# Kernel tuning notes

Measured on AMD Instinct MI355X. Metric: run time of the kernel, lower is better.

## Reference

```python
import jax, jax.numpy as jnp
import numpy as np

VOXEL_SIZE = 0.1
EPS = 1e-5  # torch BatchNorm1d default eps
P1, P2, P3 = 73856093, 19349663, 83492791  # spatial hash primes


def _bn_gelu(x, g, b):
    # BatchNorm1d in training mode (batch stats, biased variance) + exact GELU
    m = x.mean(0)
    v = ((x - m) ** 2).mean(0)
    return jax.nn.gelu(g * (x - m) * jax.lax.rsqrt(v + EPS) + b, approximate=False)


def setup_inputs() -> dict:
    key = jax.random.key(0)
    ks = jax.random.split(key, 6)
    B, N, D = 4, 65536, 128
    return {
        "points": jax.random.normal(ks[0], (B, N, 3), jnp.float32) * 4.0,
        "w1": jax.random.normal(ks[1], (3, D), jnp.float32) * (3 ** -0.5),
        "g1": jnp.ones((D,), jnp.float32), "b1": jnp.zeros((D,), jnp.float32),
        "w2": jax.random.normal(ks[2], (D, D), jnp.float32) * (D ** -0.5),
        "g2": jnp.ones((D,), jnp.float32), "b2": jnp.zeros((D,), jnp.float32),
        "w3": jax.random.normal(ks[3], (D + 6, D), jnp.float32) * ((D + 6) ** -0.5),
        "g3": jnp.ones((D,), jnp.float32), "b3": jnp.zeros((D,), jnp.float32),
        "w4": jax.random.normal(ks[4], (D, D), jnp.float32) * (D ** -0.5),
        "g4": jnp.ones((D,), jnp.float32), "b4": jnp.zeros((D,), jnp.float32),
    }


def reference(points, w1, g1, b1, w2, g2, b2, w3, g3, b3, w4, g4, b4):
    B, N, _ = points.shape
    P = B * N  # target_size in the torch module
    pts = points.reshape(P, 3)

    # --- hash-based voxel grouping (voxel_pooling_torch) ---
    vidx = jnp.floor(pts / VOXEL_SIZE).astype(jnp.int32)           # (P,3)
    vhash = vidx[:, 0] * P1 + vidx[:, 1] * P2 + vidx[:, 2] * P3    # (P,)
    _, inv = jnp.unique(vhash, return_inverse=True, size=P,
                        fill_value=jnp.iinfo(jnp.int32).min)       # inv: (P,)

    counts = jax.ops.segment_sum(jnp.ones((P,), pts.dtype), inv, num_segments=P)
    denom = jnp.maximum(counts, 1.0)[:, None]
    # scatter_reduce 'mean' over points; empty (padded) voxel slots stay 0,
    # matching pad_tensor(fill_value=0)
    voxel_centroids = jax.ops.segment_sum(pts, inv, num_segments=P) / denom  # (P,3)
    pooled_features = voxel_centroids  # features == flat_points, mean pooling

    # unique voxel coords with batch index, padded with -1 (pad_tensor fill=-1)
    batch_idx = jnp.repeat(jnp.arange(B, dtype=jnp.int32), N)
    uvox = jnp.full((P, 4), -1, jnp.int32).at[inv].set(
        jnp.concatenate([batch_idx[:, None], vidx], axis=1))
    uvox = jnp.where(counts[:, None] > 0, uvox, -1)

    # --- centroid normalization + MLPs ---
    norm_points = pts - voxel_centroids[inv]                        # (P,3)
    pe = _bn_gelu(norm_points @ w1, g1, b1)
    pos_embs = _bn_gelu(pe @ w2, g2, b2)                            # (P,D)

    concat = jnp.concatenate([pts, pos_embs, pooled_features], axis=1)  # (P,D+6)
    af = _bn_gelu(concat @ w3, g3, b3)
    aggregated = _bn_gelu(af @ w4, g4, b4)                          # (P,D)

    # sparse COO tensor represented as (indices, values)
    return aggregated, uvox.T, norm_points
```

## Files before the change

### kernel.cpp

```cpp
#include <hip/hip_runtime.h>
#include <cstddef>

#define EPSBN 1e-5f

typedef __attribute__((ext_vector_type(8))) short bf16x8;
typedef __attribute__((ext_vector_type(4))) float f32x4;

__device__ __forceinline__ float gelu_f(float x) {
    return 0.5f * x * (1.0f + erff(x * 0.70710678118654752440f));
}

__device__ __forceinline__ float bfu2f(unsigned short u) {
    unsigned v = ((unsigned)u) << 16;
    return __uint_as_float(v);
}

__device__ __forceinline__ unsigned short f2bfu(float f) {
    unsigned u = __float_as_uint(f);
    unsigned r = (u + 0x7fffu + ((u >> 16) & 1u)) >> 16;
    return (unsigned short)r;
}

__device__ __forceinline__ int swz_byte(int byte, int r) {
    return (byte < 256) ? (byte ^ ((r & 7) << 4)) : byte;
}

__device__ __forceinline__ void voxel_idx(const float* __restrict__ pts, int i,
                                          int& vx, int& vy, int& vz) {
    float x = pts[i * 3 + 0], y = pts[i * 3 + 1], z = pts[i * 3 + 2];
    vx = (int)floorf(x / 0.1f);
    vy = (int)floorf(y / 0.1f);
    vz = (int)floorf(z / 0.1f);
}

__device__ __forceinline__ unsigned flip_hash(const float* __restrict__ pts, int i) {
    int vx, vy, vz;
    voxel_idx(pts, i, vx, vy, vz);
    unsigned h = (unsigned)vx * 73856093u + (unsigned)vy * 19349663u + (unsigned)vz * 83492791u;
    return h ^ 0x80000000u;
}

__global__ void fill_f32(float* p, float v, int n) {
    int i = blockIdx.x * blockDim.x + threadIdx.x;
    if (i < n) p[i] = v;
}

__global__ void key_kernel(const float* __restrict__ pts, int* __restrict__ key,
                           int* __restrict__ cnt, int P) {
    int i = blockIdx.x * blockDim.x + threadIdx.x;
    if (i >= P) return;
    unsigned fk = flip_hash(pts, i);
    key[i] = (int)fk;
    atomicAdd(&cnt[fk >> 16], 1);
}

__global__ void scanA(const int* __restrict__ in, int* __restrict__ out, int* __restrict__ bsum) {
    __shared__ int s[256];
    int tid = threadIdx.x;
    int i = blockIdx.x * 256 + tid;
    int v = in[i];
    s[tid] = v;
    __syncthreads();
    for (int off = 1; off < 256; off <<= 1) {
        int t = (tid >= off) ? s[tid - off] : 0;
        __syncthreads();
        s[tid] += t;
        __syncthreads();
    }
    out[i] = s[tid] - v;
    if (tid == 255) bsum[blockIdx.x] = s[255];
}

__global__ void scanB(int* bsum) {
    __shared__ int s[256];
    int tid = threadIdx.x;
    int v = bsum[tid];
    s[tid] = v;
    __syncthreads();
    for (int off = 1; off < 256; off <<= 1) {
        int t = (tid >= off) ? s[tid - off] : 0;
        __syncthreads();
        s[tid] += t;
        __syncthreads();
    }
    bsum[tid] = s[tid] - v;
}

__global__ void scanC(int* __restrict__ out, const int* __restrict__ bsum) {
    out[blockIdx.x * 256 + threadIdx.x] += bsum[blockIdx.x];
}

__global__ void scatter_kernel(const int* __restrict__ key, const int* __restrict__ off,
                               int* __restrict__ fill, int* __restrict__ lo, int P) {
    int i = blockIdx.x * blockDim.x + threadIdx.x;
    if (i >= P) return;
    unsigned fk = (unsigned)key[i];
    int hi = fk >> 16;
    int pos = off[hi] + atomicAdd(&fill[hi], 1);
    lo[pos] = (int)(fk & 0xFFFFu);
}

__global__ void bucket_unique(const int* __restrict__ off, const int* __restrict__ cnt,
                              int* __restrict__ lo, int* __restrict__ dcnt, int NB) {
    int b = blockIdx.x * blockDim.x + threadIdx.x;
    if (b >= NB) return;
    int n = cnt[b];
    int base = off[b];
    if (n == 0) { dcnt[b] = 0; return; }
    for (int j = 0; j < n - 1; ++j) {
        int mi = j, mv = lo[base + j];
        for (int k = j + 1; k < n; ++k) {
            int v = lo[base + k];
            if (v < mv) { mv = v; mi = k; }
        }
        if (mi != j) { lo[base + mi] = lo[base + j]; lo[base + j] = mv; }
    }
    int d = 0, prev = -1;
    for (int j = 0; j < n; ++j) {
        int v = lo[base + j];
        if (j == 0 || v != prev) lo[base + d++] = v;
        prev = v;
    }
    dcnt[b] = d;
}

__global__ void rank_kernel(const int* __restrict__ key, const int* __restrict__ off,
                            const int* __restrict__ dcnt, const int* __restrict__ lo,
                            const int* __restrict__ dpre, int* __restrict__ inv, int P) {
    int i = blockIdx.x * blockDim.x + threadIdx.x;
    if (i >= P) return;
    unsigned fk = (unsigned)key[i];
    int hi = fk >> 16;
    int l = (int)(fk & 0xFFFFu);
    int base = off[hi];
    int d = dcnt[hi];
    int r = 0;
    for (int j = 0; j < d; ++j) {
        if (lo[base + j] == l) { r = j; break; }
    }
    inv[i] = dpre[hi] + r;
}

__global__ void accum_kernel(const float* __restrict__ pts, const int* __restrict__ inv,
                             float* __restrict__ counts, float* __restrict__ csum,
                             int* __restrict__ winner, int P) {
    int i = blockIdx.x * blockDim.x + threadIdx.x;
    if (i >= P) return;
    int s = inv[i];
    atomicAdd(&counts[s], 1.0f);
    atomicAdd(&csum[s * 3 + 0], pts[i * 3 + 0]);
    atomicAdd(&csum[s * 3 + 1], pts[i * 3 + 1]);
    atomicAdd(&csum[s * 3 + 2], pts[i * 3 + 2]);
    atomicMax(&winner[s], i);
}

__global__ void centroid_kernel(float* __restrict__ csum, const float* __restrict__ counts, int P) {
    int s = blockIdx.x * blockDim.x + threadIdx.x;
    if (s >= P) return;
    float d = fmaxf(counts[s], 1.0f);
    csum[s * 3 + 0] /= d;
    csum[s * 3 + 1] /= d;
    csum[s * 3 + 2] /= d;
}

__global__ void uvox_norm_kernel(const float* __restrict__ pts, const int* __restrict__ inv,
                                 const int* __restrict__ winner, const float* __restrict__ cent,
                                 float* __restrict__ out2, float* __restrict__ out3,
                                 int P, int N) {
    int i = blockIdx.x * blockDim.x + threadIdx.x;
    if (i >= P) return;
    int s = inv[i];
    float px = pts[i * 3 + 0], py = pts[i * 3 + 1], pz = pts[i * 3 + 2];
    out3[i * 3 + 0] = px - cent[s * 3 + 0];
    out3[i * 3 + 1] = py - cent[s * 3 + 1];
    out3[i * 3 + 2] = pz - cent[s * 3 + 2];
    if (winner[s] == i) {
        out2[0 * (size_t)P + s] = (float)(i / N);
        out2[1 * (size_t)P + s] = (float)(int)floorf(px / 0.1f);
        out2[2 * (size_t)P + s] = (float)(int)floorf(py / 0.1f);
        out2[3 * (size_t)P + s] = (float)(int)floorf(pz / 0.1f);
    }
}

__global__ void l1stats(const float* __restrict__ norm, const float* __restrict__ w1g,
                        float* __restrict__ spart, int P) {
    int c = threadIdx.x;
    int row0 = blockIdx.x * 64;
    float w0 = w1g[c], wa = w1g[128 + c], wb = w1g[256 + c];
    float s = 0.f, q = 0.f;
    for (int r = 0; r < 64; ++r) {
        const float* nr = norm + (size_t)(row0 + r) * 3;
        float v = nr[0] * w0 + nr[1] * wa + nr[2] * wb;
        s += v;
        q += v * v;
    }
    int b = blockIdx.x & 63;
    atomicAdd(&spart[b * 256 + c], s);
    atomicAdd(&spart[b * 256 + 128 + c], q);
}

__global__ void finalize_bn(const float* __restrict__ spart, const float* __restrict__ g,
                            const float* __restrict__ b, float* __restrict__ prm, int P) {
    int c = threadIdx.x;
    float s = 0.f, q = 0.f;
    for (int t = 0; t < 64; ++t) {
        s += spart[t * 256 + c];
        q += spart[t * 256 + 128 + c];
    }
    float m = s / (float)P;
    float var = fmaxf(q / (float)P - m * m, 0.f);
    float A = g[c] * rsqrtf(var + EPSBN);
    prm[c] = A;
    prm[128 + c] = b[c] - A * m;
}

__global__ void prep_wt(const float* __restrict__ w2, const float* __restrict__ w3,
                        const float* __restrict__ w4, unsigned short* __restrict__ wt2,
                        unsigned short* __restrict__ wt3, unsigned short* __restrict__ wt4) {
    int t = blockIdx.x * 256 + threadIdx.x;
    if (t < 16384) {
        int n = t >> 7, k = t & 127;
        wt2[n * 128 + k] = f2bfu(w2[k * 128 + n]);
    } else if (t < 16384 + 20480) {
        int u = t - 16384;
        int n = u / 160, k = u - n * 160;
        float v = 0.f;
        if (k < 134) {
            int r = (k < 128) ? (k + 3) : ((k < 131) ? (k - 128) : k);
            v = w3[r * 128 + n];
        }
        wt3[n * 160 + k] = f2bfu(v);
    } else if (t < 53248) {
        int u = t - 36864;
        int n = u >> 7, k = u & 127;
        wt4[n * 128 + k] = f2bfu(w4[k * 128 + n]);
    }
}

template <int KPAD, int MODE>
__launch_bounds__(256, 2)
__global__ void gemm_layer(const unsigned short* __restrict__ act_raw,
                           const float* __restrict__ norm,
                           const float* __restrict__ w1g,
                           const float* __restrict__ prm,
                           const float* __restrict__ pts,
                           const float* __restrict__ cent,
                           const unsigned short* __restrict__ wt,
                           unsigned short* __restrict__ out_raw,
                           float* __restrict__ spart, int P) {
    __shared__ __align__(16) unsigned short sA[64 * KPAD];
    const int tid = threadIdx.x;
    const int row0 = blockIdx.x * 64;

    for (int e = tid * 4; e < 64 * 128; e += 1024) {
        int r = e >> 7, k = e & 127;
        float v0, v1, v2, v3;
        if constexpr (MODE == 1) {
            const float* nr = norm + (size_t)(row0 + r) * 3;
            float n0 = nr[0], n1 = nr[1], n2 = nr[2];
            float r0 = n0 * w1g[k + 0] + n1 * w1g[128 + k + 0] + n2 * w1g[256 + k + 0];
            float r1 = n0 * w1g[k + 1] + n1 * w1g[128 + k + 1] + n2 * w1g[256 + k + 1];
            float r2 = n0 * w1g[k + 2] + n1 * w1g[128 + k + 2] + n2 * w1g[256 + k + 2];
            float r3 = n0 * w1g[k + 3] + n1 * w1g[128 + k + 3] + n2 * w1g[256 + k + 3];
            float4 pA = *(const float4*)&prm[k];
            float4 pB = *(const float4*)&prm[128 + k];
            v0 = gelu_f(pA.x * r0 + pB.x);
            v1 = gelu_f(pA.y * r1 + pB.y);
            v2 = gelu_f(pA.z * r2 + pB.z);
            v3 = gelu_f(pA.w * r3 + pB.w);
        } else {
            ushort4 rv = *(const ushort4*)&act_raw[(size_t)(row0 + r) * 128 + k];
            float4 pA = *(const float4*)&prm[k];
            float4 pB = *(const float4*)&prm[128 + k];
            v0 = gelu_f(pA.x * bfu2f(rv.x) + pB.x);
            v1 = gelu_f(pA.y * bfu2f(rv.y) + pB.y);
            v2 = gelu_f(pA.z * bfu2f(rv.z) + pB.z);
            v3 = gelu_f(pA.w * bfu2f(rv.w) + pB.w);
        }
        unsigned lo = (unsigned)f2bfu(v0) | ((unsigned)f2bfu(v1) << 16);
        unsigned hi = (unsigned)f2bfu(v2) | ((unsigned)f2bfu(v3) << 16);
        *(uint2*)((char*)sA + r * (KPAD * 2) + swz_byte(k * 2, r)) = make_uint2(lo, hi);
    }
    if constexpr (MODE == 2) {
        for (int t = tid; t < 64 * 8; t += 256) {
            int r = t >> 3, ch = t & 7;
            float a = 0.f, b = 0.f, c = 0.f, d = 0.f;
            if (ch == 0) {
                a = pts[(size_t)(row0 + r) * 3 + 0];
                b = pts[(size_t)(row0 + r) * 3 + 1];
                c = pts[(size_t)(row0 + r) * 3 + 2];
                d = cent[(size_t)(row0 + r) * 3 + 0];
            } else if (ch == 1) {
                a = cent[(size_t)(row0 + r) * 3 + 1];
                b = cent[(size_t)(row0 + r) * 3 + 2];
            }
            unsigned lo = (unsigned)f2bfu(a) | ((unsigned)f2bfu(b) << 16);
            unsigned hi = (unsigned)f2bfu(c) | ((unsigned)f2bfu(d) << 16);
            int byte = swz_byte((128 + ch * 4) * 2, r);
            *(uint2*)((char*)sA + r * (KPAD * 2) + byte) = make_uint2(lo, hi);
        }
    }
    __syncthreads();

    const int lane = tid & 63;
    const int wid = tid >> 6;
    const int lrow = lane & 15;
    const int kg = lane >> 4;

    const unsigned short* wbase = wt + (size_t)(wid * 32 + lrow) * KPAD + kg * 8;

    f32x4 acc[4][2] = {};
#pragma unroll
    for (int ks = 0; ks < KPAD / 32; ++ks) {
        bf16x8 a[4], b[2];
        int kbyte = ks * 64 + kg * 16;
#pragma unroll
        for (int j = 0; j < 2; ++j)
            b[j] = *(const bf16x8*)(wbase + (size_t)j * 16 * KPAD + ks * 32);
#pragma unroll
        for (int i = 0; i < 4; ++i) {
            int r = i * 16 + lrow;
            a[i] = *(const bf16x8*)((const char*)sA + r * (KPAD * 2) + swz_byte(kbyte, r));
        }
#pragma unroll
        for (int i = 0; i < 4; ++i)
#pragma unroll
            for (int j = 0; j < 2; ++j)
                acc[i][j] = __builtin_amdgcn_mfma_f32_16x16x32_bf16(a[i], b[j], acc[i][j], 0, 0, 0);
    }

    float s[2] = {0.f, 0.f}, q[2] = {0.f, 0.f};
#pragma unroll
    for (int i = 0; i < 4; ++i) {
        int rbase = row0 + i * 16 + kg * 4;
#pragma unroll
        for (int j = 0; j < 2; ++j) {
            int col = wid * 32 + j * 16 + lrow;
#pragma unroll
            for (int reg = 0; reg < 4; ++reg) {
                float v = acc[i][j][reg];
                out_raw[(size_t)(rbase + reg) * 128 + col] = f2bfu(v);
                s[j] += v;
                q[j] += v * v;
            }
        }
    }

    __syncthreads();
    float* red = (float*)sA;
    red[tid] = 0.f;
    __syncthreads();
#pragma unroll
    for (int j = 0; j < 2; ++j) {
        int col = wid * 32 + j * 16 + lrow;
        atomicAdd(&red[col], s[j]);
        atomicAdd(&red[128 + col], q[j]);
    }
    __syncthreads();
    atomicAdd(&spart[(blockIdx.x & 63) * 256 + tid], red[tid]);
}

__global__ void bn_gelu_out(const unsigned short* __restrict__ raw, const float* __restrict__ prm,
                            float* __restrict__ out, int n) {
    int i = blockIdx.x * blockDim.x + threadIdx.x;
    int idx4 = i * 4;
    if (idx4 >= n) return;
    ushort4 v = *(const ushort4*)&raw[idx4];
    int c = idx4 & 127;
    float4 o;
    o.x = gelu_f(prm[c + 0] * bfu2f(v.x) + prm[128 + c + 0]);
    o.y = gelu_f(prm[c + 1] * bfu2f(v.y) + prm[128 + c + 1]);
    o.z = gelu_f(prm[c + 2] * bfu2f(v.z) + prm[128 + c + 2]);
    o.w = gelu_f(prm[c + 3] * bfu2f(v.w) + prm[128 + c + 3]);
    *(float4*)&out[idx4] = o;
}

extern "C" void kernel_launch(void* const* d_in, const int* in_sizes, int n_in,
                              void* d_out, int out_size, void* d_ws, size_t ws_size,
                              hipStream_t stream) {
    const float* pts = (const float*)d_in[0];
    const float* w1 = (const float*)d_in[1];
    const float* g1 = (const float*)d_in[2];
    const float* b1 = (const float*)d_in[3];
    const float* w2 = (const float*)d_in[4];
    const float* g2 = (const float*)d_in[5];
    const float* b2 = (const float*)d_in[6];
    const float* w3 = (const float*)d_in[7];
    const float* g3 = (const float*)d_in[8];
    const float* b3 = (const float*)d_in[9];
    const float* w4 = (const float*)d_in[10];
    const float* g4 = (const float*)d_in[11];
    const float* b4 = (const float*)d_in[12];

    const int P = in_sizes[0] / 3;
    const int N = P / 4;
    const int NB = 65536;

    float* out0 = (float*)d_out;
    float* out2 = out0 + (size_t)P * 128;
    float* out3 = out2 + (size_t)P * 4;

    char* ws = (char*)d_ws;
    size_t P4 = (size_t)P * 4;
    int* d_key = (int*)(ws + 0 * P4);
    int* d_lo = (int*)(ws + 1 * P4);
    int* d_inv = (int*)(ws + 2 * P4);
    float* d_counts = (float*)(ws + 3 * P4);
    float* d_csum = (float*)(ws + 4 * P4);
    int* d_winner = (int*)(ws + 7 * P4);
    char* base8 = ws + 8 * P4;
    int* d_cnt = (int*)(base8);
    int* d_off = (int*)(base8 + 1 * 262144);
    int* d_fill = (int*)(base8 + 2 * 262144);
    int* d_dcnt = (int*)(base8 + 3 * 262144);
    int* d_dpre = (int*)(base8 + 4 * 262144);
    float* d_stats = (float*)(base8 + 5 * 262144);
    float* d_params = (float*)(base8 + 6 * 262144);
    int* d_bsum = (int*)(base8 + 6 * 262144 + 16384);
    unsigned short* d_wt2 = (unsigned short*)(base8 + 6 * 262144 + 65536);
    unsigned short* d_wt3 = d_wt2 + 128 * 128;
    unsigned short* d_wt4 = d_wt3 + 128 * 160;
    char* bufbase = base8 + 6 * 262144 + 65536 + 262144;
    unsigned short* d_bufA = (unsigned short*)bufbase;
    unsigned short* d_bufB = (unsigned short*)(bufbase + (size_t)P * 128 * 2);

    const int nb = (P + 255) / 256;

    (void)hipMemsetAsync(d_cnt, 0, 262144, stream);
    (void)hipMemsetAsync(d_fill, 0, 262144, stream);
    (void)hipMemsetAsync(d_counts, 0, P4, stream);
    (void)hipMemsetAsync(d_csum, 0, 3 * P4, stream);
    (void)hipMemsetAsync(d_winner, 0xFF, P4, stream);
    (void)hipMemsetAsync(d_stats, 0, 262144, stream);
    fill_f32<<<(4 * P + 255) / 256, 256, 0, stream>>>(out2, -1.0f, 4 * P);

    key_kernel<<<nb, 256, 0, stream>>>(pts, d_key, d_cnt, P);
    scanA<<<256, 256, 0, stream>>>(d_cnt, d_off, d_bsum);
    scanB<<<1, 256, 0, stream>>>(d_bsum);
    scanC<<<256, 256, 0, stream>>>(d_off, d_bsum);
    scatter_kernel<<<nb, 256, 0, stream>>>(d_key, d_off, d_fill, d_lo, P);
    bucket_unique<<<NB / 256, 256, 0, stream>>>(d_off, d_cnt, d_lo, d_dcnt, NB);
    scanA<<<256, 256, 0, stream>>>(d_dcnt, d_dpre, d_bsum);
    scanB<<<1, 256, 0, stream>>>(d_bsum);
    scanC<<<256, 256, 0, stream>>>(d_dpre, d_bsum);
    rank_kernel<<<nb, 256, 0, stream>>>(d_key, d_off, d_dcnt, d_lo, d_dpre, d_inv, P);

    accum_kernel<<<nb, 256, 0, stream>>>(pts, d_inv, d_counts, d_csum, d_winner, P);
    centroid_kernel<<<nb, 256, 0, stream>>>(d_csum, d_counts, P);
    uvox_norm_kernel<<<nb, 256, 0, stream>>>(pts, d_inv, d_winner, d_csum, out2, out3, P, N);

    prep_wt<<<208, 256, 0, stream>>>(w2, w3, w4, d_wt2, d_wt3, d_wt4);

    l1stats<<<P / 64, 128, 0, stream>>>(out3, w1, d_stats, P);
    finalize_bn<<<1, 128, 0, stream>>>(d_stats, g1, b1, d_params, P);

    gemm_layer<128, 1><<<P / 64, 256, 0, stream>>>(
        nullptr, out3, w1, d_params, nullptr, nullptr, d_wt2, d_bufA, d_stats + 1 * 64 * 256, P);
    finalize_bn<<<1, 128, 0, stream>>>(d_stats + 1 * 64 * 256, g2, b2, d_params + 256, P);

    gemm_layer<160, 2><<<P / 64, 256, 0, stream>>>(
        d_bufA, nullptr, nullptr, d_params + 256, pts, d_csum, d_wt3, d_bufB, d_stats + 2 * 64 * 256, P);
    finalize_bn<<<1, 128, 0, stream>>>(d_stats + 2 * 64 * 256, g3, b3, d_params + 512, P);

    gemm_layer<128, 0><<<P / 64, 256, 0, stream>>>(
        d_bufB, nullptr, nullptr, d_params + 512, nullptr, nullptr, d_wt4, d_bufA, d_stats + 3 * 64 * 256, P);
    finalize_bn<<<1, 128, 0, stream>>>(d_stats + 3 * 64 * 256, g4, b4, d_params + 768, P);

    bn_gelu_out<<<(P * 128 / 4 + 255) / 256, 256, 0, stream>>>(
        d_bufA, d_params + 768, out0, P * 128);
}
```

Baseline: 581.8 us.

## Fuse voxel preprocessing kernels and replace three-pass scans with single-block scan

Folds the -1 fill of the voxel-coordinate output into the hashing kernel, merges rank lookup with the centroid atomics, and merges centroid normalization with the layer-1 BN statistics using shared memory. The three-kernel hierarchical scans become a single 1024-thread block scan, and the separate memsets are coalesced into fewer calls. This cuts launch count and extra global round trips over the point arrays. In exchange, the single-block scan serializes 64 elements per thread, and the fused stats kernel assumes P is a multiple of 256.

```diff
diff --git a/kernel.cpp b/kernel.cpp
--- a/kernel.cpp
+++ b/kernel.cpp
@@ -25,69 +25,47 @@
     return (byte < 256) ? (byte ^ ((r & 7) << 4)) : byte;
 }
 
-__device__ __forceinline__ void voxel_idx(const float* __restrict__ pts, int i,
-                                          int& vx, int& vy, int& vz) {
-    float x = pts[i * 3 + 0], y = pts[i * 3 + 1], z = pts[i * 3 + 2];
-    vx = (int)floorf(x / 0.1f);
-    vy = (int)floorf(y / 0.1f);
-    vz = (int)floorf(z / 0.1f);
-}
-
-__device__ __forceinline__ unsigned flip_hash(const float* __restrict__ pts, int i) {
-    int vx, vy, vz;
-    voxel_idx(pts, i, vx, vy, vz);
+__device__ __forceinline__ unsigned flip_hash3(float x, float y, float z) {
+    int vx = (int)floorf(x / 0.1f);
+    int vy = (int)floorf(y / 0.1f);
+    int vz = (int)floorf(z / 0.1f);
     unsigned h = (unsigned)vx * 73856093u + (unsigned)vy * 19349663u + (unsigned)vz * 83492791u;
     return h ^ 0x80000000u;
 }
 
-__global__ void fill_f32(float* p, float v, int n) {
-    int i = blockIdx.x * blockDim.x + threadIdx.x;
-    if (i < n) p[i] = v;
-}
-
-__global__ void key_kernel(const float* __restrict__ pts, int* __restrict__ key,
-                           int* __restrict__ cnt, int P) {
+__global__ void key_fill_kernel(const float* __restrict__ pts, int* __restrict__ key,
+                                int* __restrict__ cnt, float* __restrict__ out2, int P) {
     int i = blockIdx.x * blockDim.x + threadIdx.x;
     if (i >= P) return;
-    unsigned fk = flip_hash(pts, i);
+    unsigned fk = flip_hash3(pts[i * 3 + 0], pts[i * 3 + 1], pts[i * 3 + 2]);
     key[i] = (int)fk;
     atomicAdd(&cnt[fk >> 16], 1);
-}
-
-__global__ void scanA(const int* __restrict__ in, int* __restrict__ out, int* __restrict__ bsum) {
-    __shared__ int s[256];
+    out2[0 * (size_t)P + i] = -1.0f;
+    out2[1 * (size_t)P + i] = -1.0f;
+    out2[2 * (size_t)P + i] = -1.0f;
+    out2[3 * (size_t)P + i] = -1.0f;
+}
+
+__global__ void scan_ex(const int* __restrict__ in, int* __restrict__ out, int n) {
+    __shared__ int s[1024];
     int tid = threadIdx.x;
-    int i = blockIdx.x * 256 + tid;
-    int v = in[i];
-    s[tid] = v;
-    __syncthreads();
-    for (int off = 1; off < 256; off <<= 1) {
+    int beg = tid * 64;
+    int sum = 0;
+    for (int i = 0; i < 64; ++i) sum += in[beg + i];
+    s[tid] = sum;
+    __syncthreads();
+    for (int off = 1; off < 1024; off <<= 1) {
         int t = (tid >= off) ? s[tid - off] : 0;
         __syncthreads();
         s[tid] += t;
         __syncthreads();
     }
-    out[i] = s[tid] - v;
-    if (tid == 255) bsum[blockIdx.x] = s[255];
-}
-
-__global__ void scanB(int* bsum) {
-    __shared__ int s[256];
-    int tid = threadIdx.x;
-    int v = bsum[tid];
-    s[tid] = v;
-    __syncthreads();
-    for (int off = 1; off < 256; off <<= 1) {
-        int t = (tid >= off) ? s[tid - off] : 0;
-        __syncthreads();
-        s[tid] += t;
-        __syncthreads();
-    }
-    bsum[tid] = s[tid] - v;
-}
-
-__global__ void scanC(int* __restrict__ out, const int* __restrict__ bsum) {
-    out[blockIdx.x * 256 + threadIdx.x] += bsum[blockIdx.x];
+    int base = s[tid] - sum;
+    for (int i = 0; i < 64; ++i) {
+        int v = in[beg + i];
+        out[beg + i] = base;
+        base += v;
+    }
 }
 
 __global__ void scatter_kernel(const int* __restrict__ key, const int* __restrict__ off,
@@ -124,9 +102,11 @@
     dcnt[b] = d;
 }
 
-__global__ void rank_kernel(const int* __restrict__ key, const int* __restrict__ off,
-                            const int* __restrict__ dcnt, const int* __restrict__ lo,
-                            const int* __restrict__ dpre, int* __restrict__ inv, int P) {
+__global__ void rank_accum_kernel(const int* __restrict__ key, const int* __restrict__ off,
+                                  const int* __restrict__ dcnt, const int* __restrict__ lo,
+                                  const int* __restrict__ dpre, const float* __restrict__ pts,
+                                  int* __restrict__ inv, float* __restrict__ counts,
+                                  float* __restrict__ csum, int* __restrict__ winner, int P) {
     int i = blockIdx.x * blockDim.x + threadIdx.x;
     if (i >= P) return;
     unsigned fk = (unsigned)key[i];
@@ -138,15 +118,8 @@
     for (int j = 0; j < d; ++j) {
         if (lo[base + j] == l) { r = j; break; }
     }
-    inv[i] = dpre[hi] + r;
-}
-
-__global__ void accum_kernel(const float* __restrict__ pts, const int* __restrict__ inv,
-                             float* __restrict__ counts, float* __restrict__ csum,
-                             int* __restrict__ winner, int P) {
-    int i = blockIdx.x * blockDim.x + threadIdx.x;
-    if (i >= P) return;
-    int s = inv[i];
+    int s = dpre[hi] + r;
+    inv[i] = s;
     atomicAdd(&counts[s], 1.0f);
     atomicAdd(&csum[s * 3 + 0], pts[i * 3 + 0]);
     atomicAdd(&csum[s * 3 + 1], pts[i * 3 + 1]);
@@ -163,40 +136,46 @@
     csum[s * 3 + 2] /= d;
 }
 
-__global__ void uvox_norm_kernel(const float* __restrict__ pts, const int* __restrict__ inv,
-                                 const int* __restrict__ winner, const float* __restrict__ cent,
-                                 float* __restrict__ out2, float* __restrict__ out3,
-                                 int P, int N) {
-    int i = blockIdx.x * blockDim.x + threadIdx.x;
-    if (i >= P) return;
+__global__ void uvox_norm_l1_kernel(const float* __restrict__ pts, const int* __restrict__ inv,
+                                    const int* __restrict__ winner, const float* __restrict__ cent,
+                                    const float* __restrict__ w1g, float* __restrict__ out2,
+                                    float* __restrict__ out3, float* __restrict__ spart,
+                                    int P, int N) {
+    __shared__ float sn[256 * 3];
+    int tid = threadIdx.x;
+    int i = blockIdx.x * 256 + tid;
     int s = inv[i];
     float px = pts[i * 3 + 0], py = pts[i * 3 + 1], pz = pts[i * 3 + 2];
-    out3[i * 3 + 0] = px - cent[s * 3 + 0];
-    out3[i * 3 + 1] = py - cent[s * 3 + 1];
-    out3[i * 3 + 2] = pz - cent[s * 3 + 2];
+    float n0 = px - cent[s * 3 + 0];
+    float n1 = py - cent[s * 3 + 1];
+    float n2 = pz - cent[s * 3 + 2];
+    out3[i * 3 + 0] = n0;
+    out3[i * 3 + 1] = n1;
+    out3[i * 3 + 2] = n2;
     if (winner[s] == i) {
         out2[0 * (size_t)P + s] = (float)(i / N);
         out2[1 * (size_t)P + s] = (float)(int)floorf(px / 0.1f);
         out2[2 * (size_t)P + s] = (float)(int)floorf(py / 0.1f);
         out2[3 * (size_t)P + s] = (float)(int)floorf(pz / 0.1f);
     }
-}
-
-__global__ void l1stats(const float* __restrict__ norm, const float* __restrict__ w1g,
-                        float* __restrict__ spart, int P) {
-    int c = threadIdx.x;
-    int row0 = blockIdx.x * 64;
+    sn[tid * 3 + 0] = n0;
+    sn[tid * 3 + 1] = n1;
+    sn[tid * 3 + 2] = n2;
+    __syncthreads();
+    int c = tid & 127;
+    int h = tid >> 7;
     float w0 = w1g[c], wa = w1g[128 + c], wb = w1g[256 + c];
-    float s = 0.f, q = 0.f;
-    for (int r = 0; r < 64; ++r) {
-        const float* nr = norm + (size_t)(row0 + r) * 3;
-        float v = nr[0] * w0 + nr[1] * wa + nr[2] * wb;
-        s += v;
-        q += v * v;
+    float ssum = 0.f, qsum = 0.f;
+    int r0 = h * 128;
+    for (int r = 0; r < 128; ++r) {
+        int row = r0 + r;
+        float v = sn[row * 3 + 0] * w0 + sn[row * 3 + 1] * wa + sn[row * 3 + 2] * wb;
+        ssum += v;
+        qsum += v * v;
     }
     int b = blockIdx.x & 63;
-    atomicAdd(&spart[b * 256 + c], s);
-    atomicAdd(&spart[b * 256 + 128 + c], q);
+    atomicAdd(&spart[b * 256 + c], ssum);
+    atomicAdd(&spart[b * 256 + 128 + c], qsum);
 }
 
 __global__ void finalize_bn(const float* __restrict__ spart, const float* __restrict__ g,
@@ -410,13 +389,12 @@
     int* d_winner = (int*)(ws + 7 * P4);
     char* base8 = ws + 8 * P4;
     int* d_cnt = (int*)(base8);
-    int* d_off = (int*)(base8 + 1 * 262144);
-    int* d_fill = (int*)(base8 + 2 * 262144);
+    int* d_fill = (int*)(base8 + 1 * 262144);
+    int* d_off = (int*)(base8 + 2 * 262144);
     int* d_dcnt = (int*)(base8 + 3 * 262144);
     int* d_dpre = (int*)(base8 + 4 * 262144);
     float* d_stats = (float*)(base8 + 5 * 262144);
     float* d_params = (float*)(base8 + 6 * 262144);
-    int* d_bsum = (int*)(base8 + 6 * 262144 + 16384);
     unsigned short* d_wt2 = (unsigned short*)(base8 + 6 * 262144 + 65536);
     unsigned short* d_wt3 = d_wt2 + 128 * 128;
     unsigned short* d_wt4 = d_wt3 + 128 * 160;
@@ -426,32 +404,24 @@
 
     const int nb = (P + 255) / 256;
 
-    (void)hipMemsetAsync(d_cnt, 0, 262144, stream);
-    (void)hipMemsetAsync(d_fill, 0, 262144, stream);
-    (void)hipMemsetAsync(d_counts, 0, P4, stream);
-    (void)hipMemsetAsync(d_csum, 0, 3 * P4, stream);
+    (void)hipMemsetAsync(d_cnt, 0, 2 * 262144, stream);
+    (void)hipMemsetAsync(d_counts, 0, 4 * P4, stream);
     (void)hipMemsetAsync(d_winner, 0xFF, P4, stream);
     (void)hipMemsetAsync(d_stats, 0, 262144, stream);
-    fill_f32<<<(4 * P + 255) / 256, 256, 0, stream>>>(out2, -1.0f, 4 * P);
-
-    key_kernel<<<nb, 256, 0, stream>>>(pts, d_key, d_cnt, P);
-    scanA<<<256, 256, 0, stream>>>(d_cnt, d_off, d_bsum);
-    scanB<<<1, 256, 0, stream>>>(d_bsum);
-    scanC<<<256, 256, 0, stream>>>(d_off, d_bsum);
+
+    prep_wt<<<208, 256, 0, stream>>>(w2, w3, w4, d_wt2, d_wt3, d_wt4);
+
+    key_fill_kernel<<<nb, 256, 0, stream>>>(pts, d_key, d_cnt, out2, P);
+    scan_ex<<<1, 1024, 0, stream>>>(d_cnt, d_off, NB);
     scatter_kernel<<<nb, 256, 0, stream>>>(d_key, d_off, d_fill, d_lo, P);
     bucket_unique<<<NB / 256, 256, 0, stream>>>(d_off, d_cnt, d_lo, d_dcnt, NB);
-    scanA<<<256, 256, 0, stream>>>(d_dcnt, d_dpre, d_bsum);
-    scanB<<<1, 256, 0, stream>>>(d_bsum);
-    scanC<<<256, 256, 0, stream>>>(d_dpre, d_bsum);
-    rank_kernel<<<nb, 256, 0, stream>>>(d_key, d_off, d_dcnt, d_lo, d_dpre, d_inv, P);
-
-    accum_kernel<<<nb, 256, 0, stream>>>(pts, d_inv, d_counts, d_csum, d_winner, P);
+    scan_ex<<<1, 1024, 0, stream>>>(d_dcnt, d_dpre, NB);
+    rank_accum_kernel<<<nb, 256, 0, stream>>>(d_key, d_off, d_dcnt, d_lo, d_dpre, pts,
+                                              d_inv, d_counts, d_csum, d_winner, P);
     centroid_kernel<<<nb, 256, 0, stream>>>(d_csum, d_counts, P);
-    uvox_norm_kernel<<<nb, 256, 0, stream>>>(pts, d_inv, d_winner, d_csum, out2, out3, P, N);
-
-    prep_wt<<<208, 256, 0, stream>>>(w2, w3, w4, d_wt2, d_wt3, d_wt4);
-
-    l1stats<<<P / 64, 128, 0, stream>>>(out3, w1, d_stats, P);
+
+    uvox_norm_l1_kernel<<<P / 256, 256, 0, stream>>>(pts, d_inv, d_winner, d_csum, w1,
+                                                     out2, out3, d_stats, P, N);
     finalize_bn<<<1, 128, 0, stream>>>(d_stats, g1, b1, d_params, P);
 
     gemm_layer<128, 1><<<P / 64, 256, 0, stream>>>(
```

Result: slower. 611.8 us (+5.2%).
